# Kernel optimization log

Measured on AMD Instinct MI355X. Metric: run time of the kernel, lower is better.

## Reference

```python
import jax, jax.numpy as jnp
import numpy as np

# physical / init constants (from DPINeuron.__init__ with default 1e-12 currents)
I0 = 5e-13
UT = 0.025
KAPPA = (0.75 + 0.66) / 2  # 0.705
CMEM, CAMPA, CSHUNT = 3e-12, 2e-12, 2e-12
ITAU_MEM = 1e-12
IGAIN_MEM = 1e-12
ITAU_AMPA = 1e-12
IGAIN_AMPA = 1e-12
ITH = 1e-12
IPFB_TH = 1e-12
IPFB_NORM = 1e-12
REFP = 0.0
DT = 0.001
TAU_MEM = UT / KAPPA * CMEM / ITAU_MEM
TAU_AMPA = UT / KAPPA * CAMPA / ITAU_AMPA
TAU_SHUNT = UT / KAPPA * CSHUNT / ITAU_AMPA
SLOPE = 25.0  # fast_sigmoid surrogate slope

@jax.custom_vjp
def ste_round(x):
    return jnp.round(x)

def _round_fwd(x):
    return jnp.round(x), None

def _round_bwd(_, g):
    return (g,)  # straight-through estimator

ste_round.defvjp(_round_fwd, _round_bwd)

@jax.custom_vjp
def fast_sigmoid(x):
    return (x > 0).astype(x.dtype)

def _fs_fwd(x):
    return (x > 0).astype(x.dtype), x

def _fs_bwd(x, g):
    return (g / (SLOPE * jnp.abs(x) + 1.0) ** 2,)

fast_sigmoid.defvjp(_fs_fwd, _fs_bwd)

B, N_IN, N_OUT = 4096, 2048, 2048

def setup_inputs() -> dict:
    key = jax.random.key(0)
    k1, = jax.random.split(key, 1)
    X = (jax.random.uniform(k1, (B, N_IN), dtype=jnp.float32) < 0.1).astype(jnp.float32)  # sparse input spikes
    return {
        "X": X,
        "W_ampa": jnp.ones((N_OUT, N_IN), jnp.float32),   # init.constant_(1.0)
        "W_shunt": jnp.ones((N_OUT, N_IN), jnp.float32),
        "Imem": jnp.full((B, N_OUT), I0, jnp.float32),    # initialize(): zeros + I0
        "Iampa": jnp.full((B, N_OUT), I0, jnp.float32),
        "Ishunt": jnp.full((B, N_OUT), I0, jnp.float32),
        "refractory": jnp.zeros((B, N_OUT), jnp.float32),
        "Idc": jnp.float32(1e-12),
        "Iw_ampa": jnp.float32(1e-12),
        "Iw_shunt": jnp.float32(1e-12),
        "alpha": jnp.float32(IGAIN_MEM / ITAU_MEM),       # 1.0
        "beta": jnp.float32(1.0 + I0 / ITAU_MEM),         # 1.5
    }

def reference(X, W_ampa, W_shunt, Imem, Iampa, Ishunt, refractory,
              Idc, Iw_ampa, Iw_shunt, alpha, beta):
    Iahp = I0
    Inmda = I0
    # synapse projections with STE-rounded weights: [B, n_out]
    numSynAmpa = jnp.einsum('bi,oi->bo', X, ste_round(W_ampa))
    numSynShunt = jnp.einsum('bi,oi->bo', X, ste_round(W_shunt))

    dIampa = -Iampa / TAU_AMPA
    Iampa = Iampa + (IGAIN_AMPA / ITAU_AMPA) * Iw_ampa * numSynAmpa
    dIshunt = -Ishunt / TAU_SHUNT
    Ishunt = Ishunt + (IGAIN_AMPA / ITAU_AMPA) * Iw_shunt * numSynShunt

    Iin = Idc + Iampa + Inmda - Ishunt
    Iin = Iin * (refractory <= 0)
    Iin = jnp.maximum(Iin, I0)

    Ifb = (I0 ** (1.0 / (KAPPA + 1.0))) * Imem ** (KAPPA / (KAPPA + 1.0)) \
          / (1.0 + jnp.exp(-IPFB_NORM * (Imem - IPFB_TH)))
    f_imem = Ifb / ITAU_MEM * (Imem + IGAIN_MEM)
    dImem = (alpha * (Iin - ITAU_MEM - Iahp) - beta * Imem
             + jax.lax.stop_gradient(f_imem)) / (TAU_MEM * (1.0 + IGAIN_MEM / Imem))
    Imem = jnp.maximum(Imem + dImem * DT, I0)

    # note: original code applies dIshunt decay to Iampa (kept faithful)
    Iampa = jnp.maximum(Iampa + dIampa * DT, I0)
    Iampa = jnp.maximum(Iampa + dIshunt * DT, I0)

    spike = fast_sigmoid(Imem - ITH)
    Imem = (1.0 - spike) * Imem + spike * I0
    refractory = jnp.maximum(refractory - DT, 0.0)
    refractory = (1.0 - spike) * refractory + spike * REFP
    return spike, Imem, Iampa, Ishunt, refractory
```

## Files before the change

kernel.cpp:

```cpp
#include <hip/hip_runtime.h>
#include <cmath>

#ifndef __has_builtin
#define __has_builtin(x) 0
#endif

#define B_DIM 4096
#define K_DIM 2048
#define N_DIM 2048

#define BM 128
#define BN 128
#define BK 64

typedef __attribute__((ext_vector_type(4))) float f32x4;
typedef __attribute__((ext_vector_type(8))) short bf16x8;
typedef __attribute__((ext_vector_type(8))) unsigned short u16x8;


__device__ __forceinline__ unsigned short f2bf(float f) {
    unsigned int u = __float_as_uint(f);
    u += 0x7fffu + ((u >> 16) & 1u);
    return (unsigned short)(u >> 16);
}

__device__ __forceinline__ void gl2lds16(const void* g, void* l) {
#if __has_builtin(__builtin_amdgcn_global_load_lds)
    __builtin_amdgcn_global_load_lds((__attribute__((address_space(1))) void*)g,
                                     (__attribute__((address_space(3))) void*)l,
                                     16, 0, 0);
#else
    *(uint4*)l = *(const uint4*)g;
#endif
}


__global__ void cast_x_kernel(const float* __restrict__ X,
                              unsigned short* __restrict__ Xb) {
    size_t i = ((size_t)blockIdx.x * 256 + threadIdx.x) * 8;
    f32x4 a = *(const f32x4*)(X + i);
    f32x4 b = *(const f32x4*)(X + i + 4);
    u16x8 o;
    o[0] = f2bf(a[0]); o[1] = f2bf(a[1]); o[2] = f2bf(a[2]); o[3] = f2bf(a[3]);
    o[4] = f2bf(b[0]); o[5] = f2bf(b[1]); o[6] = f2bf(b[2]); o[7] = f2bf(b[3]);
    *(u16x8*)(Xb + i) = o;
}

__global__ void cast_w_kernel(const float* __restrict__ Wa,
                              const float* __restrict__ Ws,
                              unsigned short* __restrict__ Wab,
                              unsigned short* __restrict__ Wsb) {
    size_t i = ((size_t)blockIdx.x * 256 + threadIdx.x) * 8;
    f32x4 a0 = *(const f32x4*)(Wa + i);
    f32x4 a1 = *(const f32x4*)(Wa + i + 4);
    f32x4 s0 = *(const f32x4*)(Ws + i);
    f32x4 s1 = *(const f32x4*)(Ws + i + 4);
    u16x8 oa, os;
#pragma unroll
    for (int j = 0; j < 4; j++) {
        oa[j]     = f2bf(rintf(a0[j]));
        oa[j + 4] = f2bf(rintf(a1[j]));
        os[j]     = f2bf(rintf(s0[j]));
        os[j + 4] = f2bf(rintf(s1[j]));
    }
    *(u16x8*)(Wab + i) = oa;
    *(u16x8*)(Wsb + i) = os;
}


#define RS 132

__global__ __launch_bounds__(256, 2)
void dpi_fused_kernel(const unsigned short* __restrict__ Xb,
                      const unsigned short* __restrict__ Wab,
                      const unsigned short* __restrict__ Wsb,
                      const float* __restrict__ gImem,
                      const float* __restrict__ gIampa,
                      const float* __restrict__ gIshunt,
                      const float* __restrict__ gRefr,
                      const float* __restrict__ pIdc,
                      const float* __restrict__ pIwa,
                      const float* __restrict__ pIws,
                      const float* __restrict__ pAlpha,
                      const float* __restrict__ pBeta,
                      float* __restrict__ out,
                      float i0pow, float kexp, float tau_mem, float inv_tau_syn)
{
    __shared__ __align__(16) unsigned char smem[49152];
    unsigned short* sA  = (unsigned short*)smem;
    unsigned short* sWa = (unsigned short*)(smem + 16384);
    unsigned short* sWs = (unsigned short*)(smem + 32768);
    float* na_buf = (float*)smem;
    float* ns_buf = (float*)(smem + 16896);

    const int tid  = threadIdx.x;
    const int lane = tid & 63;
    const int wave = tid >> 6;

    const int lin = blockIdx.x;
    const int xcd = lin & 7;
    const int loc = lin >> 3;
    const int mb  = (xcd & 3) * 8 + (loc & 7);
    const int nb  = (xcd >> 2) * 8 + (loc >> 3);
    const int m0  = mb * BM;
    const int n0  = nb * BN;

    const int wm = (wave & 1) * 64;
    const int wn = (wave >> 1) * 64;

    f32x4 accA[4][4], accS[4][4];
#pragma unroll
    for (int i = 0; i < 4; i++)
#pragma unroll
        for (int j = 0; j < 4; j++) { accA[i][j] = (f32x4)0.0f; accS[i][j] = (f32x4)0.0f; }

    const int frow = lane & 15;
    const int kq   = lane >> 4;
    const int swzr = frow & 7;

    for (int k0 = 0; k0 < K_DIM; k0 += BK) {
#pragma unroll
        for (int j = 0; j < 4; j++) {
            int c    = j * 256 + tid;
            int row  = c >> 3;
            int jsrc = (c & 7) ^ (row & 7);
            size_t goffA = (size_t)(m0 + row) * K_DIM + k0 + jsrc * 8;
            size_t goffW = (size_t)(n0 + row) * K_DIM + k0 + jsrc * 8;
            gl2lds16(Xb  + goffA, sA  + c * 8);
            gl2lds16(Wab + goffW, sWa + c * 8);
            gl2lds16(Wsb + goffW, sWs + c * 8);
        }
        __syncthreads();

#pragma unroll
        for (int kk = 0; kk < 2; kk++) {
            const int jb = kk * 4 + kq;
            bf16x8 af[4], ba[4], bs[4];
#pragma unroll
            for (int mi = 0; mi < 4; mi++) {
                const int rA = wm + mi * 16 + frow;
                af[mi] = *(const bf16x8*)(sA + rA * 64 + ((jb ^ swzr) * 8));
            }
#pragma unroll
            for (int ni = 0; ni < 4; ni++) {
                const int rB = wn + ni * 16 + frow;
                const int o  = rB * 64 + ((jb ^ swzr) * 8);
                ba[ni] = *(const bf16x8*)(sWa + o);
                bs[ni] = *(const bf16x8*)(sWs + o);
            }
#pragma unroll
            for (int mi = 0; mi < 4; mi++)
#pragma unroll
                for (int ni = 0; ni < 4; ni++) {
                    accA[mi][ni] = __builtin_amdgcn_mfma_f32_16x16x32_bf16(af[mi], ba[ni], accA[mi][ni], 0, 0, 0);
                    accS[mi][ni] = __builtin_amdgcn_mfma_f32_16x16x32_bf16(af[mi], bs[ni], accS[mi][ni], 0, 0, 0);
                }
        }
        __syncthreads();
    }

    const float idc   = *pIdc;
    const float iwa   = *pIwa;
    const float iws   = *pIws;
    const float alpha = *pAlpha;
    const float beta  = *pBeta;

    const size_t plane = (size_t)B_DIM * N_DIM;
    float* __restrict__ oSpike = out;
    float* __restrict__ oImem  = out + plane;
    float* __restrict__ oIampa = out + 2 * plane;
    float* __restrict__ oIsh   = out + 3 * plane;
    float* __restrict__ oRefr  = out + 4 * plane;

    const int rowgroup = wm >> 6;
    const int quad4    = (lane >> 4) << 2;
    const int cseg     = (tid & 31) * 4;
    const int rgrp     = tid >> 5;

#pragma unroll
    for (int s = 0; s < 4; s++) {
#pragma unroll
        for (int ni = 0; ni < 4; ni++) {
            const int lcol = wn + ni * 16 + (lane & 15);
#pragma unroll
            for (int r = 0; r < 4; r++) {
                const int lrow = rowgroup * 16 + quad4 + r;
                na_buf[lrow * RS + lcol] = accA[s][ni][r];
                ns_buf[lrow * RS + lcol] = accS[s][ni][r];
            }
        }
        __syncthreads();

#pragma unroll
        for (int q = 0; q < 4; q++) {
            const int lrow = rgrp * 4 + q;
            const int grow = m0 + (lrow >> 4) * 64 + s * 16 + (lrow & 15);
            const size_t idx = (size_t)grow * N_DIM + n0 + cseg;

            const f32x4 na4 = *(const f32x4*)(na_buf + lrow * RS + cseg);
            const f32x4 ns4 = *(const f32x4*)(ns_buf + lrow * RS + cseg);
            const f32x4 im4 = *(const f32x4*)(gImem   + idx);
            const f32x4 ia4 = *(const f32x4*)(gIampa  + idx);
            const f32x4 is4 = *(const f32x4*)(gIshunt + idx);
            const f32x4 rf4 = *(const f32x4*)(gRefr   + idx);

            f32x4 sp_o, im_o, ia_o, is_o, rf_o;
#pragma unroll
            for (int e = 0; e < 4; e++) {
                const float na  = na4[e];
                const float ns  = ns4[e];
                const float im  = im4[e];
                const float ia  = ia4[e];
                const float ish = is4[e];
                const float rf  = rf4[e];

                const float dIampa  = -ia * inv_tau_syn;
                const float ia2     = ia + iwa * na;
                const float dIshunt = -ish * inv_tau_syn;
                const float ish2    = ish + iws * ns;

                float Iin = idc + ia2 + 5e-13f - ish2;
                Iin = (rf <= 0.0f) ? Iin : 0.0f;
                Iin = fmaxf(Iin, 5e-13f);

                const float ifb = i0pow *
                    __builtin_amdgcn_exp2f(kexp * __builtin_amdgcn_logf(im)) * 0.5f;
                const float fimem = ifb * 1e12f * (im + 1e-12f);
                const float dImem = (alpha * ((Iin - 1e-12f) - 5e-13f) - beta * im + fimem)
                                    / (tau_mem * (1.0f + 1e-12f / im));
                float im2 = fmaxf(im + dImem * 0.001f, 5e-13f);

                float ia3 = fmaxf(ia2 + dIampa * 0.001f, 5e-13f);
                ia3       = fmaxf(ia3 + dIshunt * 0.001f, 5e-13f);

                const float spike = (im2 - 1e-12f > 0.0f) ? 1.0f : 0.0f;
                im2 = (spike > 0.0f) ? 5e-13f : im2;
                float rf2 = fmaxf(rf - 0.001f, 0.0f);
                rf2 = (spike > 0.0f) ? 0.0f : rf2;

                sp_o[e] = spike; im_o[e] = im2; ia_o[e] = ia3;
                is_o[e] = ish2;  rf_o[e] = rf2;
            }

            *(f32x4*)(oSpike + idx) = sp_o;
            *(f32x4*)(oImem  + idx) = im_o;
            *(f32x4*)(oIampa + idx) = ia_o;
            *(f32x4*)(oIsh   + idx) = is_o;
            *(f32x4*)(oRefr  + idx) = rf_o;
        }
        __syncthreads();
    }
}


extern "C" void kernel_launch(void* const* d_in, const int* in_sizes, int n_in,
                              void* d_out, int out_size, void* d_ws, size_t ws_size,
                              hipStream_t stream) {
    (void)in_sizes; (void)n_in; (void)out_size; (void)ws_size;

    const float* X       = (const float*)d_in[0];
    const float* W_ampa  = (const float*)d_in[1];
    const float* W_shunt = (const float*)d_in[2];
    const float* Imem    = (const float*)d_in[3];
    const float* Iampa   = (const float*)d_in[4];
    const float* Ishunt  = (const float*)d_in[5];
    const float* Refr    = (const float*)d_in[6];
    const float* pIdc    = (const float*)d_in[7];
    const float* pIwa    = (const float*)d_in[8];
    const float* pIws    = (const float*)d_in[9];
    const float* pAlpha  = (const float*)d_in[10];
    const float* pBeta   = (const float*)d_in[11];

    unsigned short* Xb  = (unsigned short*)d_ws;
    unsigned short* Wab = Xb  + (size_t)B_DIM * K_DIM;
    unsigned short* Wsb = Wab + (size_t)N_DIM * K_DIM;

    const float i0pow       = (float)std::pow(5e-13, 1.0 / 1.705);
    const float kexp        = (float)(0.705 / 1.705);
    const float tau_mem     = (float)(0.025 / 0.705 * 3.0);
    const float inv_tau_syn = (float)(1.0 / (0.025 / 0.705 * 2.0));

    cast_x_kernel<<<dim3((B_DIM * K_DIM) / (256 * 8)), dim3(256), 0, stream>>>(X, Xb);
    cast_w_kernel<<<dim3((N_DIM * K_DIM) / (256 * 8)), dim3(256), 0, stream>>>(
        W_ampa, W_shunt, Wab, Wsb);

    dpi_fused_kernel<<<dim3(512), dim3(256), 0, stream>>>(
        Xb, Wab, Wsb, Imem, Iampa, Ishunt, Refr,
        pIdc, pIwa, pIws, pAlpha, pBeta,
        (float*)d_out, i0pow, kexp, tau_mem, inv_tau_syn);
}
```

Before: 369.3 us.

## Shrink N tile to 32 for higher occupancy and use nontemporal epilogue I/O

The GEMM tile shrinks from 128x128 to 128x32. The grid grows from 512 to 2048 blocks, shared memory drops to 24 KB and launch bounds target 6 blocks per CU, so more waves can hide latency and the many CUs are filled better. Each wave now holds 4 accumulator tiles per matrix instead of 16, which cuts register pressure. The epilogue's state loads and output stores switch to nontemporal hints to reduce cache pollution. The cost is that the X tile is reloaded four times as often, so arithmetic intensity per byte fetched into LDS drops.

```diff
diff --git a/kernel.cpp b/kernel.cpp
--- a/kernel.cpp
+++ b/kernel.cpp
@@ -10,7 +10,7 @@
 #define N_DIM 2048
 
 #define BM 128
-#define BN 128
+#define BN 32
 #define BK 64
 
 typedef __attribute__((ext_vector_type(4))) float f32x4;
@@ -68,9 +68,9 @@
 }
 
 
-#define RS 132
-
-__global__ __launch_bounds__(256, 2)
+#define RS 36
+
+__global__ __launch_bounds__(256, 6)
 void dpi_fused_kernel(const unsigned short* __restrict__ Xb,
                       const unsigned short* __restrict__ Wab,
                       const unsigned short* __restrict__ Wsb,
@@ -86,12 +86,12 @@
                       float* __restrict__ out,
                       float i0pow, float kexp, float tau_mem, float inv_tau_syn)
 {
-    __shared__ __align__(16) unsigned char smem[49152];
+    __shared__ __align__(16) unsigned char smem[24576];
     unsigned short* sA  = (unsigned short*)smem;
     unsigned short* sWa = (unsigned short*)(smem + 16384);
-    unsigned short* sWs = (unsigned short*)(smem + 32768);
+    unsigned short* sWs = (unsigned short*)(smem + 20480);
     float* na_buf = (float*)smem;
-    float* ns_buf = (float*)(smem + 16896);
+    float* ns_buf = (float*)(smem + 4608);
 
     const int tid  = threadIdx.x;
     const int lane = tid & 63;
@@ -101,22 +101,23 @@
     const int xcd = lin & 7;
     const int loc = lin >> 3;
     const int mb  = (xcd & 3) * 8 + (loc & 7);
-    const int nb  = (xcd >> 2) * 8 + (loc >> 3);
+    const int nb  = (xcd >> 2) * 32 + (loc >> 3);
     const int m0  = mb * BM;
     const int n0  = nb * BN;
 
     const int wm = (wave & 1) * 64;
-    const int wn = (wave >> 1) * 64;
-
-    f32x4 accA[4][4], accS[4][4];
-#pragma unroll
-    for (int i = 0; i < 4; i++)
-#pragma unroll
-        for (int j = 0; j < 4; j++) { accA[i][j] = (f32x4)0.0f; accS[i][j] = (f32x4)0.0f; }
+    const int wn = (wave >> 1) * 16;
+
+    f32x4 accA[4], accS[4];
+#pragma unroll
+    for (int i = 0; i < 4; i++) { accA[i] = (f32x4)0.0f; accS[i] = (f32x4)0.0f; }
 
     const int frow = lane & 15;
     const int kq   = lane >> 4;
     const int swzr = frow & 7;
+
+    const int rB    = wn + frow;
+    const int wbase = rB * 64;
 
     for (int k0 = 0; k0 < K_DIM; k0 += BK) {
 #pragma unroll
@@ -124,37 +125,32 @@
             int c    = j * 256 + tid;
             int row  = c >> 3;
             int jsrc = (c & 7) ^ (row & 7);
-            size_t goffA = (size_t)(m0 + row) * K_DIM + k0 + jsrc * 8;
+            gl2lds16(Xb + (size_t)(m0 + row) * K_DIM + k0 + jsrc * 8, sA + c * 8);
+        }
+        {
+            int row  = tid >> 3;
+            int jsrc = (tid & 7) ^ (row & 7);
             size_t goffW = (size_t)(n0 + row) * K_DIM + k0 + jsrc * 8;
-            gl2lds16(Xb  + goffA, sA  + c * 8);
-            gl2lds16(Wab + goffW, sWa + c * 8);
-            gl2lds16(Wsb + goffW, sWs + c * 8);
+            gl2lds16(Wab + goffW, sWa + tid * 8);
+            gl2lds16(Wsb + goffW, sWs + tid * 8);
         }
         __syncthreads();
 
 #pragma unroll
         for (int kk = 0; kk < 2; kk++) {
             const int jb = kk * 4 + kq;
-            bf16x8 af[4], ba[4], bs[4];
+            const int ko = (jb ^ swzr) * 8;
+            bf16x8 af[4];
+#pragma unroll
+            for (int mi = 0; mi < 4; mi++)
+                af[mi] = *(const bf16x8*)(sA + (wm + mi * 16 + frow) * 64 + ko);
+            const bf16x8 ba = *(const bf16x8*)(sWa + wbase + ko);
+            const bf16x8 bs = *(const bf16x8*)(sWs + wbase + ko);
 #pragma unroll
             for (int mi = 0; mi < 4; mi++) {
-                const int rA = wm + mi * 16 + frow;
-                af[mi] = *(const bf16x8*)(sA + rA * 64 + ((jb ^ swzr) * 8));
+                accA[mi] = __builtin_amdgcn_mfma_f32_16x16x32_bf16(af[mi], ba, accA[mi], 0, 0, 0);
+                accS[mi] = __builtin_amdgcn_mfma_f32_16x16x32_bf16(af[mi], bs, accS[mi], 0, 0, 0);
             }
-#pragma unroll
-            for (int ni = 0; ni < 4; ni++) {
-                const int rB = wn + ni * 16 + frow;
-                const int o  = rB * 64 + ((jb ^ swzr) * 8);
-                ba[ni] = *(const bf16x8*)(sWa + o);
-                bs[ni] = *(const bf16x8*)(sWs + o);
-            }
-#pragma unroll
-            for (int mi = 0; mi < 4; mi++)
-#pragma unroll
-                for (int ni = 0; ni < 4; ni++) {
-                    accA[mi][ni] = __builtin_amdgcn_mfma_f32_16x16x32_bf16(af[mi], ba[ni], accA[mi][ni], 0, 0, 0);
-                    accS[mi][ni] = __builtin_amdgcn_mfma_f32_16x16x32_bf16(af[mi], bs[ni], accS[mi][ni], 0, 0, 0);
-                }
         }
         __syncthreads();
     }
@@ -174,35 +170,30 @@
 
     const int rowgroup = wm >> 6;
     const int quad4    = (lane >> 4) << 2;
-    const int cseg     = (tid & 31) * 4;
-    const int rgrp     = tid >> 5;
+    const int lcol     = wn + (lane & 15);
+    const int cseg     = (tid & 7) * 4;
+    const int trow     = tid >> 3;
 
 #pragma unroll
     for (int s = 0; s < 4; s++) {
 #pragma unroll
-        for (int ni = 0; ni < 4; ni++) {
-            const int lcol = wn + ni * 16 + (lane & 15);
-#pragma unroll
-            for (int r = 0; r < 4; r++) {
-                const int lrow = rowgroup * 16 + quad4 + r;
-                na_buf[lrow * RS + lcol] = accA[s][ni][r];
-                ns_buf[lrow * RS + lcol] = accS[s][ni][r];
-            }
-        }
-        __syncthreads();
-
-#pragma unroll
-        for (int q = 0; q < 4; q++) {
-            const int lrow = rgrp * 4 + q;
-            const int grow = m0 + (lrow >> 4) * 64 + s * 16 + (lrow & 15);
+        for (int r = 0; r < 4; r++) {
+            const int lrow = rowgroup * 16 + quad4 + r;
+            na_buf[lrow * RS + lcol] = accA[s][r];
+            ns_buf[lrow * RS + lcol] = accS[s][r];
+        }
+        __syncthreads();
+
+        {
+            const int grow = m0 + (trow >> 4) * 64 + s * 16 + (trow & 15);
             const size_t idx = (size_t)grow * N_DIM + n0 + cseg;
 
-            const f32x4 na4 = *(const f32x4*)(na_buf + lrow * RS + cseg);
-            const f32x4 ns4 = *(const f32x4*)(ns_buf + lrow * RS + cseg);
-            const f32x4 im4 = *(const f32x4*)(gImem   + idx);
-            const f32x4 ia4 = *(const f32x4*)(gIampa  + idx);
-            const f32x4 is4 = *(const f32x4*)(gIshunt + idx);
-            const f32x4 rf4 = *(const f32x4*)(gRefr   + idx);
+            const f32x4 na4 = *(const f32x4*)(na_buf + trow * RS + cseg);
+            const f32x4 ns4 = *(const f32x4*)(ns_buf + trow * RS + cseg);
+            const f32x4 im4 = __builtin_nontemporal_load((const f32x4*)(gImem   + idx));
+            const f32x4 ia4 = __builtin_nontemporal_load((const f32x4*)(gIampa  + idx));
+            const f32x4 is4 = __builtin_nontemporal_load((const f32x4*)(gIshunt + idx));
+            const f32x4 rf4 = __builtin_nontemporal_load((const f32x4*)(gRefr   + idx));
 
             f32x4 sp_o, im_o, ia_o, is_o, rf_o;
 #pragma unroll
@@ -242,11 +233,11 @@
                 is_o[e] = ish2;  rf_o[e] = rf2;
             }
 
-            *(f32x4*)(oSpike + idx) = sp_o;
-            *(f32x4*)(oImem  + idx) = im_o;
-            *(f32x4*)(oIampa + idx) = ia_o;
-            *(f32x4*)(oIsh   + idx) = is_o;
-            *(f32x4*)(oRefr  + idx) = rf_o;
+            __builtin_nontemporal_store(sp_o, (f32x4*)(oSpike + idx));
+            __builtin_nontemporal_store(im_o, (f32x4*)(oImem  + idx));
+            __builtin_nontemporal_store(ia_o, (f32x4*)(oIampa + idx));
+            __builtin_nontemporal_store(is_o, (f32x4*)(oIsh   + idx));
+            __builtin_nontemporal_store(rf_o, (f32x4*)(oRefr  + idx));
         }
         __syncthreads();
     }
@@ -284,7 +275,7 @@
     cast_w_kernel<<<dim3((N_DIM * K_DIM) / (256 * 8)), dim3(256), 0, stream>>>(
         W_ampa, W_shunt, Wab, Wsb);
 
-    dpi_fused_kernel<<<dim3(512), dim3(256), 0, stream>>>(
+    dpi_fused_kernel<<<dim3((B_DIM / BM) * (N_DIM / BN)), dim3(256), 0, stream>>>(
         Xb, Wab, Wsb, Imem, Iampa, Ishunt, Refr,
         pIdc, pIwa, pIws, pAlpha, pBeta,
         (float*)d_out, i0pow, kexp, tau_mem, inv_tau_syn);
```

New measurement: 407.5 us. 10.4% more time.
